# Performance work log

Hardware: AMD Instinct MI355X
Metric: run time of the kernel (lower is better)

The kernel has to match this reference:

```python
import jax, jax.numpy as jnp
import numpy as np

N = 50000          # nodes
E = 1600000        # edges
H = 8              # heads
F = 16             # out feats per head (np1class)
IN = 256           # in feats
NEG_SLOPE = 0.2    # DGL GATConv default leaky_relu slope


def setup_inputs() -> dict:
    key = jax.random.key(0)
    ks = jax.random.split(key, 7)
    x = jax.random.normal(ks[0], (N, IN), dtype=jnp.float32)
    W = jax.random.normal(ks[1], (IN, H * F), dtype=jnp.float32) * 0.05
    attn_l = jax.random.normal(ks[2], (H, F), dtype=jnp.float32) * 0.05
    attn_r = jax.random.normal(ks[3], (H, F), dtype=jnp.float32) * 0.05
    bias = jax.random.normal(ks[4], (H * F,), dtype=jnp.float32) * 0.05
    src = jax.random.randint(ks[5], (E,), 0, N, dtype=jnp.int64)
    dst = jax.random.randint(ks[6], (E,), 0, N, dtype=jnp.int64)
    return {"x": x, "W": W, "attn_l": attn_l, "attn_r": attn_r,
            "bias": bias, "src": src, "dst": dst}


def reference(x, W, attn_l, attn_r, bias, src, dst):
    # Linear projection to heads: [N, H, F]
    feat = (x @ W).reshape(N, H, F)
    # Per-node attention halves: [N, H]
    el = jnp.einsum('nhf,hf->nh', feat, attn_l)
    er = jnp.einsum('nhf,hf->nh', feat, attn_r)
    # Edge scores: e = leaky_relu(el[src] + er[dst])  -> [E, H]
    e = jax.nn.leaky_relu(el[src] + er[dst], negative_slope=NEG_SLOPE)
    # Segment softmax over incoming edges of each destination node
    m = jax.ops.segment_max(e, dst, num_segments=N)           # [N, H]
    m = jnp.where(jnp.isfinite(m), m, 0.0)                    # empty segments
    m = jax.lax.stop_gradient(m)
    ex = jnp.exp(e - m[dst])                                  # [E, H]
    s = jax.ops.segment_sum(ex, dst, num_segments=N)          # [N, H]
    a = ex / jnp.maximum(s[dst], 1e-9)                        # [E, H]
    # Weighted aggregation of source features: [N, H, F]
    msg = a[:, :, None] * feat[src]
    rst = jax.ops.segment_sum(msg, dst, num_segments=N)
    rst = rst + bias.reshape(H, F)
    # Classifier: mean over heads -> [N, F]
    return rst.mean(axis=1)
```

## Files before the change

### kernel.cpp

```cpp
#include <hip/hip_runtime.h>
#include <hip/hip_bf16.h>

#define NH 8
#define NF 16
#define NIN 256
#define HF 128
#define CAP 3072
#define BCH 4096

typedef __attribute__((ext_vector_type(8))) short bf16x8;
typedef __attribute__((ext_vector_type(4))) float f32x4;

__device__ __forceinline__ unsigned short f2bf(float f) {
    union { float f; unsigned int u; } v; v.f = f;
    unsigned int r = v.u + 0x7FFFu + ((v.u >> 16) & 1u);
    return (unsigned short)(r >> 16);
}
__device__ __forceinline__ float bf2f(unsigned short b) {
    union { unsigned int u; float f; } v; v.u = ((unsigned int)b) << 16;
    return v.f;
}

struct GemmLds {
    unsigned short AsH[32][264];
    unsigned short AsL[32][264];
    float scratch[32][132];
};
struct CsrLds {
    unsigned int eary[CAP];
    unsigned short sSrc[CAP];
    unsigned short roff[512];
    unsigned short rcntl[512];
    int rbase[512];
    int len[64], cur[64];
    unsigned int wsum[4];
    unsigned int sbase;
};
#define POOLSZ ((sizeof(GemmLds) > sizeof(CsrLds)) ? sizeof(GemmLds) : sizeof(CsrLds))

#define GROWS 128
__device__ __forceinline__ void gemm_body(char* pool, int bid,
                                          const float* __restrict__ A,
                                          const float* __restrict__ W,
                                          const float* __restrict__ attn_l,
                                          const float* __restrict__ attn_r,
                                          unsigned short* __restrict__ featb,
                                          float* __restrict__ el,
                                          float* __restrict__ er, int M) {
    GemmLds& gl = *reinterpret_cast<GemmLds*>(pool);
    const int tid = threadIdx.x;
    const int wave = tid >> 6, lane = tid & 63;
    const int quad = lane >> 4, lq = lane & 15;
    const int row0 = bid * GROWS;

    bf16x8 bfrag[8][2];
#pragma unroll
    for (int h2 = 0; h2 < 2; h2++) {
        const int col = (wave * 2 + h2) * 16 + lq;
#pragma unroll
        for (int kk = 0; kk < 8; kk++) {
            const int kb = kk * 32 + quad * 8;
            bf16x8 f;
#pragma unroll
            for (int j = 0; j < 8; j++)
                f[j] = (short)f2bf(W[(size_t)(kb + j) * HF + col]);
            bfrag[kk][h2] = f;
        }
    }

    const int srow = tid >> 3;
    const int erow = tid >> 3, eh = tid & 7;

    for (int c = 0; c < 4; c++) {
        const int crow0 = row0 + c * 32;
        __syncthreads();
#pragma unroll
        for (int i = 0; i < 8; i++) {
            const int col = ((tid & 7) + i * 8) * 4;
            const int gr = crow0 + srow;
            float4 v = make_float4(0.f, 0.f, 0.f, 0.f);
            if (gr < M) v = *(const float4*)&A[(size_t)gr * NIN + col];
            const unsigned short h0 = f2bf(v.x), h1 = f2bf(v.y),
                                 h2b = f2bf(v.z), h3 = f2bf(v.w);
            *(ushort4*)&gl.AsH[srow][col] = make_ushort4(h0, h1, h2b, h3);
            *(ushort4*)&gl.AsL[srow][col] =
                make_ushort4(f2bf(v.x - bf2f(h0)), f2bf(v.y - bf2f(h1)),
                             f2bf(v.z - bf2f(h2b)), f2bf(v.w - bf2f(h3)));
        }
        __syncthreads();
#pragma unroll
        for (int s = 0; s < 2; s++) {
            f32x4 acc0 = {0.f, 0.f, 0.f, 0.f};
            f32x4 acc1 = {0.f, 0.f, 0.f, 0.f};
            const int ar = s * 16 + lq;
#pragma unroll
            for (int kk = 0; kk < 8; kk++) {
                const bf16x8 ah = *(const bf16x8*)&gl.AsH[ar][kk * 32 + quad * 8];
                const bf16x8 al = *(const bf16x8*)&gl.AsL[ar][kk * 32 + quad * 8];
                acc0 = __builtin_amdgcn_mfma_f32_16x16x32_bf16(ah, bfrag[kk][0], acc0, 0, 0, 0);
                acc1 = __builtin_amdgcn_mfma_f32_16x16x32_bf16(ah, bfrag[kk][1], acc1, 0, 0, 0);
                acc0 = __builtin_amdgcn_mfma_f32_16x16x32_bf16(al, bfrag[kk][0], acc0, 0, 0, 0);
                acc1 = __builtin_amdgcn_mfma_f32_16x16x32_bf16(al, bfrag[kk][1], acc1, 0, 0, 0);
            }
#pragma unroll
            for (int r = 0; r < 4; r++) {
                const int gr = crow0 + s * 16 + quad * 4 + r;
                const int srw = s * 16 + quad * 4 + r;
                gl.scratch[srw][(wave * 2 + 0) * 16 + lq] = acc0[r];
                gl.scratch[srw][(wave * 2 + 1) * 16 + lq] = acc1[r];
                if (gr < M) {
                    featb[(size_t)gr * HF + (wave * 2 + 0) * 16 + lq] = f2bf(acc0[r]);
                    featb[(size_t)gr * HF + (wave * 2 + 1) * 16 + lq] = f2bf(acc1[r]);
                }
            }
        }
        __syncthreads();
        {
            const int gr = crow0 + erow;
            if (gr < M) {
                const float* sr = &gl.scratch[erow][eh * 16];
                float sl = 0.f, srr = 0.f;
#pragma unroll
                for (int f = 0; f < 16; f++) {
                    const float v = sr[f];
                    sl = fmaf(v, attn_l[eh * 16 + f], sl);
                    srr = fmaf(v, attn_r[eh * 16 + f], srr);
                }
                el[(size_t)gr * NH + eh] = sl;
                er[(size_t)gr * NH + eh] = srr;
            }
        }
    }
}

__device__ __forceinline__ void csr_body(char* pool, int b,
                                         const unsigned int* __restrict__ binned,
                                         const unsigned int* __restrict__ runtab,
                                         int* __restrict__ nodeinfo,
                                         unsigned short* __restrict__ srcsw,
                                         int N, int NB, int nbb) {
    CsrLds& cl = *reinterpret_cast<CsrLds*>(pool);
    const int t = threadIdx.x;
    const int node0 = b << 6;
    const int lane = t & 63, w = t >> 6;
    if (t == 0) cl.sbase = 0;
    __syncthreads();
    for (int c0 = 0; c0 < nbb; c0 += 256) {
        const int r = c0 + t;
        const unsigned int e = (r < nbb) ? runtab[(size_t)r * NB + b] : 0;
        const unsigned int v = e >> 16;
        unsigned int incl = v;
#pragma unroll
        for (int off = 1; off < 64; off <<= 1) {
            const unsigned int x = __shfl_up(incl, off, 64);
            if (lane >= off) incl += x;
        }
        if (lane == 63) cl.wsum[w] = incl;
        __syncthreads();
        unsigned int wbase = 0;
        for (int k = 0; k < w; k++) wbase += cl.wsum[k];
        const unsigned int tot = cl.wsum[0] + cl.wsum[1] + cl.wsum[2] + cl.wsum[3];
        if (r < nbb) {
            cl.roff[r] = (unsigned short)(e & 0xFFFFu);
            cl.rcntl[r] = (unsigned short)v;
            cl.rbase[r] = (int)(cl.sbase + wbase + incl - v);
        }
        __syncthreads();
        if (t == 0) cl.sbase += tot;
        __syncthreads();
    }
    const int tot = (int)cl.sbase;
    for (int r = t; r < nbb; r += 256) {
        const int off = (int)cl.roff[r];
        const int pb = cl.rbase[r];
        const int rc = (int)cl.rcntl[r];
        const unsigned int* bp = &binned[(size_t)r * BCH + off];
        for (int j = 0; j < rc; j++) cl.eary[pb + j] = bp[j];
    }
    if (t < 64) cl.len[t] = 0;
    __syncthreads();
    for (int i = t; i < tot; i += 256) atomicAdd(&cl.len[cl.eary[i] >> 16], 1);
    __syncthreads();
    if (t < 64) {
        const int v = cl.len[t];
        int incl = v;
#pragma unroll
        for (int off = 1; off < 64; off <<= 1) {
            const int x = __shfl_up(incl, off, 64);
            if (t >= off) incl += x;
        }
        const int excl = incl - v;
        cl.cur[t] = excl;
        if (node0 + t < N) nodeinfo[node0 + t] = excl | (v << 16);
    }
    __syncthreads();
    for (int i = t; i < tot; i += 256) {
        const unsigned int p = cl.eary[i];
        const int pos = atomicAdd(&cl.cur[p >> 16], 1);
        cl.sSrc[pos] = (unsigned short)(p & 0xFFFFu);
    }
    __syncthreads();
    unsigned short* sw = &srcsw[(size_t)b * CAP];
    for (int i = t; i < tot; i += 256) sw[i] = cl.sSrc[i];
}

__global__ __launch_bounds__(256) void gemm_csr(const float* __restrict__ A,
                                                const float* __restrict__ W,
                                                const float* __restrict__ attn_l,
                                                const float* __restrict__ attn_r,
                                                unsigned short* __restrict__ featb,
                                                float* __restrict__ el,
                                                float* __restrict__ er, int M,
                                                const unsigned int* __restrict__ binned,
                                                const unsigned int* __restrict__ runtab,
                                                int* __restrict__ nodeinfo,
                                                unsigned short* __restrict__ srcsw,
                                                int NB, int nbb, int GB) {
    __shared__ __align__(16) char pool[POOLSZ];
    if ((int)blockIdx.x < GB)
        gemm_body(pool, blockIdx.x, A, W, attn_l, attn_r, featb, el, er, M);
    else
        csr_body(pool, blockIdx.x - GB, binned, runtab, nodeinfo, srcsw, M, NB, nbb);
}

__global__ __launch_bounds__(256) void bin_kernel(const int* __restrict__ src,
                                                  const int* __restrict__ dst,
                                                  unsigned int* __restrict__ binned,
                                                  unsigned int* __restrict__ runtab,
                                                  int E, int NB) {
    __shared__ unsigned int hist[784];
    __shared__ unsigned int offs[784];
    __shared__ unsigned short lpos[BCH];
    __shared__ unsigned int obuf[BCH];
    __shared__ int dcache[BCH];
    __shared__ unsigned int wsum[4];
    __shared__ unsigned int sbase;
    const int blk = blockIdx.x, t = threadIdx.x;
    const int base = blk * BCH;
    const int cnt = min(BCH, E - base);
    const int lane = t & 63, w = t >> 6;
    for (int b = t; b < NB; b += 256) hist[b] = 0;
    for (int i = t; i < cnt; i += 256) dcache[i] = dst[base + i];
    if (t == 0) sbase = 0;
    __syncthreads();
    for (int i = t; i < cnt; i += 256)
        lpos[i] = (unsigned short)atomicAdd(&hist[dcache[i] >> 6], 1u);
    __syncthreads();
    for (int c0 = 0; c0 < NB; c0 += 256) {
        const int idx = c0 + t;
        const unsigned int v = (idx < NB) ? hist[idx] : 0;
        unsigned int incl = v;
#pragma unroll
        for (int off = 1; off < 64; off <<= 1) {
            const unsigned int x = __shfl_up(incl, off, 64);
            if (lane >= off) incl += x;
        }
        if (lane == 63) wsum[w] = incl;
        __syncthreads();
        unsigned int wbase = 0;
        for (int k = 0; k < w; k++) wbase += wsum[k];
        const unsigned int tot = wsum[0] + wsum[1] + wsum[2] + wsum[3];
        const unsigned int excl = sbase + wbase + incl - v;
        if (idx < NB) {
            offs[idx] = excl;
            runtab[(size_t)blk * NB + idx] = excl | (v << 16);
        }
        __syncthreads();
        if (t == 0) sbase += tot;
        __syncthreads();
    }
    for (int i = t; i < cnt; i += 256) {
        const int d = dcache[i];
        obuf[offs[d >> 6] + lpos[i]] =
            (unsigned int)src[base + i] | ((unsigned int)(d & 63) << 16);
    }
    __syncthreads();
    for (int i = t; i < cnt; i += 256) binned[(size_t)base + i] = obuf[i];
}

#define WIN 64
__global__ __launch_bounds__(256) void agg_kernel(const int* __restrict__ nodeinfo,
                                                  const unsigned short* __restrict__ srcsw,
                                                  const float* __restrict__ el,
                                                  const float* __restrict__ er,
                                                  const unsigned short* __restrict__ featb,
                                                  const float* __restrict__ bias,
                                                  float* __restrict__ out, int N) {
    __shared__ float lds_sc[4][WIN][8];
    __shared__ int lds_src[4][WIN];
    const int tid = threadIdx.x;
    const int w = tid >> 6, lane = tid & 63;
    const int n = blockIdx.x * 4 + w;
    if (n >= N) return;

    const int info = nodeinfo[n];
    const int begin = (n >> 6) * CAP + (info & 0xFFFF);
    const int end = begin + (info >> 16);
    const int hA = lane & 7, eA = lane >> 3;
    const float er_h = er[(size_t)n * NH + hA];
    const int hB = lane >> 3, fB2 = lane & 7;

    float2 acc = make_float2(0.f, 0.f);
    float psum = 0.f;
    for (int base = begin; base < end; base += WIN) {
        const int cn = min(WIN, end - base);
        __builtin_amdgcn_wave_barrier();
#pragma unroll
        for (int rep = 0; rep < 8; rep++) {
            const int ei = rep * 8 + eA;
            if (ei < cn) {
                const int si = (int)srcsw[base + ei];
                if (hA == 0) lds_src[w][ei] = si;
                float v = el[(size_t)si * NH + hA] + er_h;
                v = v > 0.f ? v : 0.2f * v;
                const float sc = __expf(v);
                lds_sc[w][ei][hA] = sc;
                psum += sc;
            }
        }
        __builtin_amdgcn_wave_barrier();
        for (int b0 = 0; b0 < cn; b0 += 16) {
            unsigned int fv[16];
#pragma unroll
            for (int j = 0; j < 16; j++) {
                const int ej = b0 + j;
                const int sj = lds_src[w][ej];
                fv[j] = (ej < cn)
                            ? *(const unsigned int*)&featb[(size_t)sj * HF + hB * 16 + fB2 * 2]
                            : 0u;
            }
#pragma unroll
            for (int j = 0; j < 16; j++) {
                const int ej = b0 + j;
                const float sc = (ej < cn) ? lds_sc[w][ej][hB] : 0.f;
                acc.x = fmaf(sc, bf2f((unsigned short)(fv[j] & 0xFFFFu)), acc.x);
                acc.y = fmaf(sc, bf2f((unsigned short)(fv[j] >> 16)), acc.y);
            }
        }
    }

    float s = psum;
    s += __shfl_xor(s, 8, 64);
    s += __shfl_xor(s, 16, 64);
    s += __shfl_xor(s, 32, 64);
    const float s_h = __shfl(s, hB, 64);
    const float inv = 1.f / fmaxf(s_h, 1e-9f);
    float2 val;
    val.x = acc.x * inv + bias[hB * 16 + fB2 * 2];
    val.y = acc.y * inv + bias[hB * 16 + fB2 * 2 + 1];
    val.x += __shfl_xor(val.x, 8, 64);
    val.x += __shfl_xor(val.x, 16, 64);
    val.x += __shfl_xor(val.x, 32, 64);
    val.y += __shfl_xor(val.y, 8, 64);
    val.y += __shfl_xor(val.y, 16, 64);
    val.y += __shfl_xor(val.y, 32, 64);
    if (lane < 8) {
        float2 o;
        o.x = val.x * 0.125f;
        o.y = val.y * 0.125f;
        *(float2*)&out[(size_t)n * 16 + lane * 2] = o;
    }
}

extern "C" void kernel_launch(void* const* d_in, const int* in_sizes, int n_in,
                              void* d_out, int out_size, void* d_ws, size_t ws_size,
                              hipStream_t stream) {
    const float* x      = (const float*)d_in[0];
    const float* W      = (const float*)d_in[1];
    const float* attn_l = (const float*)d_in[2];
    const float* attn_r = (const float*)d_in[3];
    const float* bias   = (const float*)d_in[4];
    const int*   src    = (const int*)d_in[5];
    const int*   dst    = (const int*)d_in[6];
    float* out = (float*)d_out;

    const int N = in_sizes[0] / NIN;
    const int E = in_sizes[5];
    const int NB = (N + 63) >> 6;
    const int nbb = (E + BCH - 1) / BCH;
    const int GB = (N + GROWS - 1) / GROWS;

    char* w = (char*)d_ws;
    unsigned short* featb = (unsigned short*)w; w += (size_t)N * HF * 2;
    float* el     = (float*)w; w += (size_t)N * NH * 4;
    float* er     = (float*)w; w += (size_t)N * NH * 4;
    int* nodeinfo = (int*)w;   w += (size_t)N * 4;
    unsigned int* binned = (unsigned int*)w; w += (size_t)nbb * BCH * 4;
    unsigned int* runtab = (unsigned int*)w; w += (size_t)nbb * NB * 4;
    unsigned short* srcsw = (unsigned short*)w;

    bin_kernel<<<nbb, 256, 0, stream>>>(src, dst, binned, runtab, E, NB);
    gemm_csr<<<GB + NB, 256, 0, stream>>>(x, W, attn_l, attn_r, featb, el, er, N,
                                          binned, runtab, nodeinfo, srcsw, NB, nbb, GB);
    agg_kernel<<<(N + 3) / 4, 256, 0, stream>>>(nodeinfo, srcsw, el, er, featb, bias,
                                                out, N);
}
```

Measured before the change: 210.7 us.

## Split bf16 features into head-half arrays and aggregate per head half

Result: slower. 221.6 us (+5.2%).

```diff
diff --git a/kernel.cpp b/kernel.cpp
--- a/kernel.cpp
+++ b/kernel.cpp
@@ -44,7 +44,8 @@
                                           const float* __restrict__ W,
                                           const float* __restrict__ attn_l,
                                           const float* __restrict__ attn_r,
-                                          unsigned short* __restrict__ featb,
+                                          unsigned short* __restrict__ featbA,
+                                          unsigned short* __restrict__ featbB,
                                           float* __restrict__ el,
                                           float* __restrict__ er, int M) {
     GemmLds& gl = *reinterpret_cast<GemmLds*>(pool);
@@ -70,6 +71,8 @@
 
     const int srow = tid >> 3;
     const int erow = tid >> 3, eh = tid & 7;
+    unsigned short* fbp = (wave < 2) ? featbA : featbB;
+    const int cA = (wave * 2) * 16 + lq - ((wave < 2) ? 0 : 64);
 
     for (int c = 0; c < 4; c++) {
         const int crow0 = row0 + c * 32;
@@ -109,8 +112,8 @@
                 gl.scratch[srw][(wave * 2 + 0) * 16 + lq] = acc0[r];
                 gl.scratch[srw][(wave * 2 + 1) * 16 + lq] = acc1[r];
                 if (gr < M) {
-                    featb[(size_t)gr * HF + (wave * 2 + 0) * 16 + lq] = f2bf(acc0[r]);
-                    featb[(size_t)gr * HF + (wave * 2 + 1) * 16 + lq] = f2bf(acc1[r]);
+                    fbp[(size_t)gr * 64 + cA] = f2bf(acc0[r]);
+                    fbp[(size_t)gr * 64 + cA + 16] = f2bf(acc1[r]);
                 }
             }
         }
@@ -208,7 +211,8 @@
                                                 const float* __restrict__ W,
                                                 const float* __restrict__ attn_l,
                                                 const float* __restrict__ attn_r,
-                                                unsigned short* __restrict__ featb,
+                                                unsigned short* __restrict__ featbA,
+                                                unsigned short* __restrict__ featbB,
                                                 float* __restrict__ el,
                                                 float* __restrict__ er, int M,
                                                 const unsigned int* __restrict__ binned,
@@ -218,7 +222,7 @@
                                                 int NB, int nbb, int GB) {
     __shared__ __align__(16) char pool[POOLSZ];
     if ((int)blockIdx.x < GB)
-        gemm_body(pool, blockIdx.x, A, W, attn_l, attn_r, featb, el, er, M);
+        gemm_body(pool, blockIdx.x, A, W, attn_l, attn_r, featbA, featbB, el, er, M);
     else
         csr_body(pool, blockIdx.x - GB, binned, runtab, nodeinfo, srcsw, M, NB, nbb);
 }
@@ -283,22 +287,25 @@
                                                   const unsigned short* __restrict__ srcsw,
                                                   const float* __restrict__ el,
                                                   const float* __restrict__ er,
-                                                  const unsigned short* __restrict__ featb,
+                                                  const unsigned short* __restrict__ featbA,
+                                                  const unsigned short* __restrict__ featbB,
                                                   const float* __restrict__ bias,
                                                   float* __restrict__ out, int N) {
-    __shared__ float lds_sc[4][WIN][8];
+    __shared__ float lds_sc[4][WIN][4];
     __shared__ int lds_src[4][WIN];
     const int tid = threadIdx.x;
     const int w = tid >> 6, lane = tid & 63;
-    const int n = blockIdx.x * 4 + w;
+    const int hh = blockIdx.x & 1;
+    const int n = (blockIdx.x >> 1) * 4 + w;
     if (n >= N) return;
+    const unsigned short* __restrict__ fbH = hh ? featbB : featbA;
 
     const int info = nodeinfo[n];
     const int begin = (n >> 6) * CAP + (info & 0xFFFF);
     const int end = begin + (info >> 16);
-    const int hA = lane & 7, eA = lane >> 3;
-    const float er_h = er[(size_t)n * NH + hA];
-    const int hB = lane >> 3, fB2 = lane & 7;
+    const int hA = lane & 3, eA = lane >> 2;
+    const float er_h = er[(size_t)n * NH + hh * 4 + hA];
+    const int fp = lane & 7, hh2 = (lane >> 3) & 3, e1 = lane >> 5;
 
     float2 acc = make_float2(0.f, 0.f);
     float psum = 0.f;
@@ -306,12 +313,12 @@
         const int cn = min(WIN, end - base);
         __builtin_amdgcn_wave_barrier();
 #pragma unroll
-        for (int rep = 0; rep < 8; rep++) {
-            const int ei = rep * 8 + eA;
+        for (int rep = 0; rep < 4; rep++) {
+            const int ei = rep * 16 + eA;
             if (ei < cn) {
                 const int si = (int)srcsw[base + ei];
                 if (hA == 0) lds_src[w][ei] = si;
-                float v = el[(size_t)si * NH + hA] + er_h;
+                float v = el[(size_t)si * NH + hh * 4 + hA] + er_h;
                 v = v > 0.f ? v : 0.2f * v;
                 const float sc = __expf(v);
                 lds_sc[w][ei][hA] = sc;
@@ -319,20 +326,20 @@
             }
         }
         __builtin_amdgcn_wave_barrier();
-        for (int b0 = 0; b0 < cn; b0 += 16) {
+        for (int b0 = 0; b0 < cn; b0 += 32) {
             unsigned int fv[16];
 #pragma unroll
             for (int j = 0; j < 16; j++) {
-                const int ej = b0 + j;
+                const int ej = b0 + j * 2 + e1;
                 const int sj = lds_src[w][ej];
                 fv[j] = (ej < cn)
-                            ? *(const unsigned int*)&featb[(size_t)sj * HF + hB * 16 + fB2 * 2]
+                            ? *(const unsigned int*)&fbH[(size_t)sj * 64 + hh2 * 16 + fp * 2]
                             : 0u;
             }
 #pragma unroll
             for (int j = 0; j < 16; j++) {
-                const int ej = b0 + j;
-                const float sc = (ej < cn) ? lds_sc[w][ej][hB] : 0.f;
+                const int ej = b0 + j * 2 + e1;
+                const float sc = (ej < cn) ? lds_sc[w][ej][hh2] : 0.f;
                 acc.x = fmaf(sc, bf2f((unsigned short)(fv[j] & 0xFFFFu)), acc.x);
                 acc.y = fmaf(sc, bf2f((unsigned short)(fv[j] >> 16)), acc.y);
             }
@@ -340,25 +347,30 @@
     }
 
     float s = psum;
+    s += __shfl_xor(s, 4, 64);
     s += __shfl_xor(s, 8, 64);
     s += __shfl_xor(s, 16, 64);
     s += __shfl_xor(s, 32, 64);
-    const float s_h = __shfl(s, hB, 64);
+    const float s_h = __shfl(s, hh2, 64);
     const float inv = 1.f / fmaxf(s_h, 1e-9f);
+    acc.x += __shfl_xor(acc.x, 32, 64);
+    acc.y += __shfl_xor(acc.y, 32, 64);
     float2 val;
-    val.x = acc.x * inv + bias[hB * 16 + fB2 * 2];
-    val.y = acc.y * inv + bias[hB * 16 + fB2 * 2 + 1];
+    val.x = acc.x * inv;
+    val.y = acc.y * inv;
     val.x += __shfl_xor(val.x, 8, 64);
     val.x += __shfl_xor(val.x, 16, 64);
-    val.x += __shfl_xor(val.x, 32, 64);
     val.y += __shfl_xor(val.y, 8, 64);
     val.y += __shfl_xor(val.y, 16, 64);
-    val.y += __shfl_xor(val.y, 32, 64);
     if (lane < 8) {
-        float2 o;
-        o.x = val.x * 0.125f;
-        o.y = val.y * 0.125f;
-        *(float2*)&out[(size_t)n * 16 + lane * 2] = o;
+        float b0s = 0.f, b1s = 0.f;
+#pragma unroll
+        for (int h = 0; h < 4; h++) {
+            b0s += bias[(hh * 4 + h) * 16 + lane * 2];
+            b1s += bias[(hh * 4 + h) * 16 + lane * 2 + 1];
+        }
+        atomicAdd(&out[(size_t)n * 16 + lane * 2], (val.x + b0s) * 0.125f);
+        atomicAdd(&out[(size_t)n * 16 + lane * 2 + 1], (val.y + b1s) * 0.125f);
     }
 }
 
@@ -381,7 +393,8 @@
     const int GB = (N + GROWS - 1) / GROWS;
 
     char* w = (char*)d_ws;
-    unsigned short* featb = (unsigned short*)w; w += (size_t)N * HF * 2;
+    unsigned short* featbA = (unsigned short*)w; w += (size_t)N * 64 * 2;
+    unsigned short* featbB = (unsigned short*)w; w += (size_t)N * 64 * 2;
     float* el     = (float*)w; w += (size_t)N * NH * 4;
     float* er     = (float*)w; w += (size_t)N * NH * 4;
     int* nodeinfo = (int*)w;   w += (size_t)N * 4;
@@ -389,9 +402,11 @@
     unsigned int* runtab = (unsigned int*)w; w += (size_t)nbb * NB * 4;
     unsigned short* srcsw = (unsigned short*)w;
 
+    hipMemsetAsync(out, 0, (size_t)N * 16 * 4, stream);
     bin_kernel<<<nbb, 256, 0, stream>>>(src, dst, binned, runtab, E, NB);
-    gemm_csr<<<GB + NB, 256, 0, stream>>>(x, W, attn_l, attn_r, featb, el, er, N,
-                                          binned, runtab, nodeinfo, srcsw, NB, nbb, GB);
-    agg_kernel<<<(N + 3) / 4, 256, 0, stream>>>(nodeinfo, srcsw, el, er, featb, bias,
-                                                out, N);
-}
+    gemm_csr<<<GB + NB, 256, 0, stream>>>(x, W, attn_l, attn_r, featbA, featbB,
+                                          el, er, N, binned, runtab, nodeinfo,
+                                          srcsw, NB, nbb, GB);
+    agg_kernel<<<2 * ((N + 3) / 4), 256, 0, stream>>>(nodeinfo, srcsw, el, er,
+                                                      featbA, featbB, bias, out, N);
+}
```

## Replace block-local binning with global atomic bucketing by destination group

Applied to the files above, without the earlier changes.

Result: slower. 580.1 us (+175.3%).

```diff
diff --git a/kernel.cpp b/kernel.cpp
--- a/kernel.cpp
+++ b/kernel.cpp
@@ -6,7 +6,6 @@
 #define NIN 256
 #define HF 128
 #define CAP 3072
-#define BCH 4096
 
 typedef __attribute__((ext_vector_type(8))) short bf16x8;
 typedef __attribute__((ext_vector_type(4))) float f32x4;
@@ -29,12 +28,7 @@
 struct CsrLds {
     unsigned int eary[CAP];
     unsigned short sSrc[CAP];
-    unsigned short roff[512];
-    unsigned short rcntl[512];
-    int rbase[512];
     int len[64], cur[64];
-    unsigned int wsum[4];
-    unsigned int sbase;
 };
 #define POOLSZ ((sizeof(GemmLds) > sizeof(CsrLds)) ? sizeof(GemmLds) : sizeof(CsrLds))
 
@@ -134,52 +128,22 @@
 }
 
 __device__ __forceinline__ void csr_body(char* pool, int b,
-                                         const unsigned int* __restrict__ binned,
-                                         const unsigned int* __restrict__ runtab,
+                                         const unsigned int* __restrict__ bedges,
+                                         const unsigned int* __restrict__ gcount,
                                          int* __restrict__ nodeinfo,
-                                         unsigned short* __restrict__ srcsw,
-                                         int N, int NB, int nbb) {
+                                         unsigned short* __restrict__ srcsw, int N) {
     CsrLds& cl = *reinterpret_cast<CsrLds*>(pool);
     const int t = threadIdx.x;
     const int node0 = b << 6;
-    const int lane = t & 63, w = t >> 6;
-    if (t == 0) cl.sbase = 0;
-    __syncthreads();
-    for (int c0 = 0; c0 < nbb; c0 += 256) {
-        const int r = c0 + t;
-        const unsigned int e = (r < nbb) ? runtab[(size_t)r * NB + b] : 0;
-        const unsigned int v = e >> 16;
-        unsigned int incl = v;
-#pragma unroll
-        for (int off = 1; off < 64; off <<= 1) {
-            const unsigned int x = __shfl_up(incl, off, 64);
-            if (lane >= off) incl += x;
-        }
-        if (lane == 63) cl.wsum[w] = incl;
-        __syncthreads();
-        unsigned int wbase = 0;
-        for (int k = 0; k < w; k++) wbase += cl.wsum[k];
-        const unsigned int tot = cl.wsum[0] + cl.wsum[1] + cl.wsum[2] + cl.wsum[3];
-        if (r < nbb) {
-            cl.roff[r] = (unsigned short)(e & 0xFFFFu);
-            cl.rcntl[r] = (unsigned short)v;
-            cl.rbase[r] = (int)(cl.sbase + wbase + incl - v);
-        }
-        __syncthreads();
-        if (t == 0) cl.sbase += tot;
-        __syncthreads();
-    }
-    const int tot = (int)cl.sbase;
-    for (int r = t; r < nbb; r += 256) {
-        const int off = (int)cl.roff[r];
-        const int pb = cl.rbase[r];
-        const int rc = (int)cl.rcntl[r];
-        const unsigned int* bp = &binned[(size_t)r * BCH + off];
-        for (int j = 0; j < rc; j++) cl.eary[pb + j] = bp[j];
-    }
+    const int cnt = (int)gcount[b];
     if (t < 64) cl.len[t] = 0;
     __syncthreads();
-    for (int i = t; i < tot; i += 256) atomicAdd(&cl.len[cl.eary[i] >> 16], 1);
+    const unsigned int* bp = &bedges[(size_t)b * CAP];
+    for (int i = t; i < cnt; i += 256) {
+        const unsigned int p = bp[i];
+        cl.eary[i] = p;
+        atomicAdd(&cl.len[p >> 16], 1);
+    }
     __syncthreads();
     if (t < 64) {
         const int v = cl.len[t];
@@ -194,14 +158,14 @@
         if (node0 + t < N) nodeinfo[node0 + t] = excl | (v << 16);
     }
     __syncthreads();
-    for (int i = t; i < tot; i += 256) {
+    for (int i = t; i < cnt; i += 256) {
         const unsigned int p = cl.eary[i];
         const int pos = atomicAdd(&cl.cur[p >> 16], 1);
         cl.sSrc[pos] = (unsigned short)(p & 0xFFFFu);
     }
     __syncthreads();
     unsigned short* sw = &srcsw[(size_t)b * CAP];
-    for (int i = t; i < tot; i += 256) sw[i] = cl.sSrc[i];
+    for (int i = t; i < cnt; i += 256) sw[i] = cl.sSrc[i];
 }
 
 __global__ __launch_bounds__(256) void gemm_csr(const float* __restrict__ A,
@@ -211,71 +175,31 @@
                                                 unsigned short* __restrict__ featb,
                                                 float* __restrict__ el,
                                                 float* __restrict__ er, int M,
-                                                const unsigned int* __restrict__ binned,
-                                                const unsigned int* __restrict__ runtab,
+                                                const unsigned int* __restrict__ bedges,
+                                                const unsigned int* __restrict__ gcount,
                                                 int* __restrict__ nodeinfo,
                                                 unsigned short* __restrict__ srcsw,
-                                                int NB, int nbb, int GB) {
+                                                int GB) {
     __shared__ __align__(16) char pool[POOLSZ];
     if ((int)blockIdx.x < GB)
         gemm_body(pool, blockIdx.x, A, W, attn_l, attn_r, featb, el, er, M);
     else
-        csr_body(pool, blockIdx.x - GB, binned, runtab, nodeinfo, srcsw, M, NB, nbb);
+        csr_body(pool, blockIdx.x - GB, bedges, gcount, nodeinfo, srcsw, M);
 }
 
 __global__ __launch_bounds__(256) void bin_kernel(const int* __restrict__ src,
                                                   const int* __restrict__ dst,
-                                                  unsigned int* __restrict__ binned,
-                                                  unsigned int* __restrict__ runtab,
-                                                  int E, int NB) {
-    __shared__ unsigned int hist[784];
-    __shared__ unsigned int offs[784];
-    __shared__ unsigned short lpos[BCH];
-    __shared__ unsigned int obuf[BCH];
-    __shared__ int dcache[BCH];
-    __shared__ unsigned int wsum[4];
-    __shared__ unsigned int sbase;
-    const int blk = blockIdx.x, t = threadIdx.x;
-    const int base = blk * BCH;
-    const int cnt = min(BCH, E - base);
-    const int lane = t & 63, w = t >> 6;
-    for (int b = t; b < NB; b += 256) hist[b] = 0;
-    for (int i = t; i < cnt; i += 256) dcache[i] = dst[base + i];
-    if (t == 0) sbase = 0;
-    __syncthreads();
-    for (int i = t; i < cnt; i += 256)
-        lpos[i] = (unsigned short)atomicAdd(&hist[dcache[i] >> 6], 1u);
-    __syncthreads();
-    for (int c0 = 0; c0 < NB; c0 += 256) {
-        const int idx = c0 + t;
-        const unsigned int v = (idx < NB) ? hist[idx] : 0;
-        unsigned int incl = v;
-#pragma unroll
-        for (int off = 1; off < 64; off <<= 1) {
-            const unsigned int x = __shfl_up(incl, off, 64);
-            if (lane >= off) incl += x;
-        }
-        if (lane == 63) wsum[w] = incl;
-        __syncthreads();
-        unsigned int wbase = 0;
-        for (int k = 0; k < w; k++) wbase += wsum[k];
-        const unsigned int tot = wsum[0] + wsum[1] + wsum[2] + wsum[3];
-        const unsigned int excl = sbase + wbase + incl - v;
-        if (idx < NB) {
-            offs[idx] = excl;
-            runtab[(size_t)blk * NB + idx] = excl | (v << 16);
-        }
-        __syncthreads();
-        if (t == 0) sbase += tot;
-        __syncthreads();
-    }
-    for (int i = t; i < cnt; i += 256) {
-        const int d = dcache[i];
-        obuf[offs[d >> 6] + lpos[i]] =
-            (unsigned int)src[base + i] | ((unsigned int)(d & 63) << 16);
-    }
-    __syncthreads();
-    for (int i = t; i < cnt; i += 256) binned[(size_t)base + i] = obuf[i];
+                                                  unsigned int* __restrict__ bedges,
+                                                  unsigned int* __restrict__ gcount,
+                                                  int E) {
+    const int stride = gridDim.x * 256;
+    for (int i = blockIdx.x * 256 + threadIdx.x; i < E; i += stride) {
+        const int d = dst[i];
+        const int b = d >> 6;
+        const unsigned int pos = atomicAdd(&gcount[b], 1u);
+        bedges[(size_t)b * CAP + pos] =
+            (unsigned int)src[i] | ((unsigned int)(d & 63) << 16);
+    }
 }
 
 #define WIN 64
@@ -377,7 +301,6 @@
     const int N = in_sizes[0] / NIN;
     const int E = in_sizes[5];
     const int NB = (N + 63) >> 6;
-    const int nbb = (E + BCH - 1) / BCH;
     const int GB = (N + GROWS - 1) / GROWS;
 
     char* w = (char*)d_ws;
@@ -385,13 +308,14 @@
     float* el     = (float*)w; w += (size_t)N * NH * 4;
     float* er     = (float*)w; w += (size_t)N * NH * 4;
     int* nodeinfo = (int*)w;   w += (size_t)N * 4;
-    unsigned int* binned = (unsigned int*)w; w += (size_t)nbb * BCH * 4;
-    unsigned int* runtab = (unsigned int*)w; w += (size_t)nbb * NB * 4;
+    unsigned int* bedges = (unsigned int*)w; w += (size_t)NB * CAP * 4;
+    unsigned int* gcount = (unsigned int*)w; w += (size_t)NB * 4;
     unsigned short* srcsw = (unsigned short*)w;
 
-    bin_kernel<<<nbb, 256, 0, stream>>>(src, dst, binned, runtab, E, NB);
+    hipMemsetAsync(gcount, 0, (size_t)NB * 4, stream);
+    bin_kernel<<<2048, 256, 0, stream>>>(src, dst, bedges, gcount, E);
     gemm_csr<<<GB + NB, 256, 0, stream>>>(x, W, attn_l, attn_r, featb, el, er, N,
-                                          binned, runtab, nodeinfo, srcsw, NB, nbb, GB);
+                                          bedges, gcount, nodeinfo, srcsw, GB);
     agg_kernel<<<(N + 3) / 4, 256, 0, stream>>>(nodeinfo, srcsw, el, er, featb, bias,
                                                 out, N);
 }
```
